# Kernel optimization log

Hardware: AMD Instinct MI355X
Metric: run time of the kernel (lower is better)

Reference implementation:

```python
import jax, jax.numpy as jnp
import numpy as np

VOCAB, E, HIDDEN = 100000, 64, (64, 128, 64)
B, T = 4096, 200


def setup_inputs() -> dict:
    key = jax.random.key(0)
    ks = jax.random.split(key, 12)
    # glorot-ish scales
    def glorot(k, shape):
        fan_in, fan_out = shape[0], shape[-1]
        s = jnp.sqrt(6.0 / (fan_in + fan_out))
        return jax.random.uniform(k, shape, jnp.float32, -s, s)
    return {
        "query": jax.random.randint(ks[0], (B,), 0, VOCAB),
        "keys": jax.random.randint(ks[1], (B, T), 0, VOCAB),
        "emb": glorot(ks[2], (VOCAB, E)),
        "att_w1": glorot(ks[3], (4 * E, 64)),
        "att_b1": jnp.zeros((64,), jnp.float32),
        "att_w2": glorot(ks[4], (64, 1)),
        "att_b2": jnp.zeros((1,), jnp.float32),
        "deep_w1": glorot(ks[5], (HIDDEN[0], HIDDEN[1])),
        "deep_b1": jnp.zeros((HIDDEN[1],), jnp.float32),
        "deep_w2": glorot(ks[6], (HIDDEN[1], HIDDEN[2])),
        "deep_b2": jnp.zeros((HIDDEN[2],), jnp.float32),
        "out_w": glorot(ks[7], (HIDDEN[2], 1)),
        "out_b": jnp.zeros((1,), jnp.float32),
    }


def reference(query, keys, emb, att_w1, att_b1, att_w2, att_b2,
              deep_w1, deep_b1, deep_w2, deep_b2, out_w, out_b):
    q = emb[query]                # [B, E]
    k = emb[keys]                 # [B, T, E]
    qe = jnp.broadcast_to(q[:, None, :], k.shape)  # [B, T, E]
    inter = jnp.concatenate([qe, k, qe - k, qe * k], axis=-1)  # [B, T, 4E]
    h = jax.nn.relu(inter @ att_w1 + att_b1)       # [B, T, 64]
    scores = (h @ att_w2 + att_b2)[..., 0]         # [B, T]
    w = jax.nn.softmax(scores, axis=-1)            # [B, T]
    interest = jnp.einsum("bt,bte->be", w, k)      # [B, E]
    d = jax.nn.relu(interest @ deep_w1 + deep_b1)
    d = jax.nn.relu(d @ deep_w2 + deep_b2)
    return jax.nn.sigmoid(d @ out_w + out_b)       # [B, 1]
```

## Files before the change

### kernel.cpp

```cpp
#include <hip/hip_runtime.h>

#define T 200
#define E 64
#define TPAD 256
#define ROW 72
#define BDIM 256
#define TP 208

typedef __bf16 bf16_t;
typedef __bf16 bf16x8 __attribute__((ext_vector_type(8)));
typedef float f32x4 __attribute__((ext_vector_type(4)));

__global__ __launch_bounds__(256) void pre_cvt(const float* __restrict__ embf,
                                               bf16_t* __restrict__ emb16, int n8,
                                               const float* __restrict__ w1,
                                               float* __restrict__ Ap,
                                               float* __restrict__ Ctf,
                                               float* __restrict__ Dtf) {
    const int bid = blockIdx.x;
    if (bid < 16) {
        const int idx = bid * 256 + threadIdx.x;
        const int e = idx >> 6, j = idx & 63;
        const float a = w1[e * 64 + j];
        const float b = w1[(64 + e) * 64 + j];
        const float c = w1[(128 + e) * 64 + j];
        const float d = w1[(192 + e) * 64 + j];
        Ap[e * 64 + j]  = a + c;
        Ctf[j * 64 + e] = b - c;
        Dtf[j * 64 + e] = d;
        return;
    }
    const int i = (bid - 16) * 256 + threadIdx.x;
    if (i >= n8) return;
    const float4* s = (const float4*)embf + (size_t)i * 2;
    const float4 a = s[0], b = s[1];
    union { bf16_t h[8]; uint4 v; } u;
    u.h[0] = (bf16_t)a.x; u.h[1] = (bf16_t)a.y; u.h[2] = (bf16_t)a.z; u.h[3] = (bf16_t)a.w;
    u.h[4] = (bf16_t)b.x; u.h[5] = (bf16_t)b.y; u.h[6] = (bf16_t)b.z; u.h[7] = (bf16_t)b.w;
    ((uint4*)emb16)[i] = u.v;
}

__global__ __launch_bounds__(256, 4) void din_fast(
    const int* __restrict__ query,
    const int* __restrict__ keys,
    const bf16_t* __restrict__ emb16,
    const float* __restrict__ Ap,
    const float* __restrict__ Ctf,
    const float* __restrict__ Dtf,
    const float* __restrict__ b1,
    const float* __restrict__ w2,
    const float* __restrict__ b2,
    const float* __restrict__ dw1,
    const float* __restrict__ db1,
    const float* __restrict__ dw2,
    const float* __restrict__ db2,
    const float* __restrict__ ow,
    const float* __restrict__ ob,
    float* __restrict__ out)
{
    __shared__ __align__(16) char smem[39936];
    bf16_t* sK   = (bf16_t*)smem;
    bf16_t* sMt  = (bf16_t*)(smem + 29952);
    float*  sUP  = (float*)(smem + 39168);
    float*  sQf  = (float*)(smem + 39680);
    float*  sWgt = (float*)(smem + 29952);
    float*  sRed = (float*)(smem + 30784);
    float*  sInt = (float*)(smem + 30816);
    float*  sD1  = (float*)(smem + 31072);
    float*  sD2  = (float*)(smem + 31584);
    float*  sIP  = (float*)(smem + 31840);

    const int tid  = threadIdx.x;
    const int lane = tid & 63;
    const int wid  = tid >> 6;
    const int b    = blockIdx.x;
    const float b2v = b2[0];

    const int c8    = tid & 7;
    const int rbase = tid >> 3;
    uint4 kr[7];
    #pragma unroll
    for (int i = 0; i < 7; ++i) {
        const int t = rbase + 32 * i;
        if (t < T) {
            const int ki = keys[b * T + t];
            kr[i] = ((const uint4*)(emb16 + (size_t)ki * E))[c8];
        } else {
            kr[i] = make_uint4(0u, 0u, 0u, 0u);
        }
    }

    const int qi = query[b];
    if (tid < 64) sQf[tid] = (float)emb16[(size_t)qi * E + tid];
    __syncthreads();

    if (tid < 128) {
        const int j = tid & 63, ec = tid >> 6;
        float au = 0.f;
        #pragma unroll
        for (int eo = 0; eo < 32; ++eo) {
            const int e = ec * 32 + eo;
            au = fmaf(sQf[e], Ap[e * 64 + j], au);
        }
        sUP[tid] = au;
    }
    {
        const int j = tid & 63, h = tid >> 6;
        const float* cp = Ctf + j * 64 + h * 16;
        const float* dp = Dtf + j * 64 + h * 16;
        const float* qp = sQf + h * 16;
        bf16_t mo[16] __attribute__((aligned(16)));
        #pragma unroll
        for (int x = 0; x < 16; ++x)
            mo[x] = (bf16_t)fmaf(qp[x], dp[x], cp[x]);
        *(bf16x8*)&sMt[j * ROW + h * 16]     = *(bf16x8*)&mo[0];
        *(bf16x8*)&sMt[j * ROW + h * 16 + 8] = *(bf16x8*)&mo[8];
    }
    __syncthreads();

    #pragma unroll
    for (int i = 0; i < 7; ++i) {
        const int t = rbase + 32 * i;
        if (t < TP) *(uint4*)&sK[t * ROW + c8 * 8] = kr[i];
    }
    __syncthreads();

    {
        const int n    = lane & 15;
        const int quad = lane >> 4;
        float w2v[4], uv[4];
        bf16x8 bF[4][2];
        #pragma unroll
        for (int nt = 0; nt < 4; ++nt) {
            const int jj = nt * 16 + n;
            w2v[nt] = w2[jj];
            uv[nt]  = b1[jj] + sUP[jj] + sUP[64 + jj];
            bF[nt][0] = *(const bf16x8*)&sMt[jj * ROW + quad * 8];
            bF[nt][1] = *(const bf16x8*)&sMt[jj * ROW + 32 + quad * 8];
        }
        __syncthreads();

        for (int mt = wid; mt < 13; mt += 4) {
            const bf16x8 a0 = *(const bf16x8*)&sK[(mt * 16 + n) * ROW + quad * 8];
            const bf16x8 a1 = *(const bf16x8*)&sK[(mt * 16 + n) * ROW + 32 + quad * 8];
            float s0 = 0.f, s1 = 0.f, s2 = 0.f, s3 = 0.f;
            #pragma unroll
            for (int nt = 0; nt < 4; ++nt) {
                f32x4 acc = { uv[nt], uv[nt], uv[nt], uv[nt] };
                acc = __builtin_amdgcn_mfma_f32_16x16x32_bf16(a0, bF[nt][0], acc, 0, 0, 0);
                acc = __builtin_amdgcn_mfma_f32_16x16x32_bf16(a1, bF[nt][1], acc, 0, 0, 0);
                s0 = fmaf(fmaxf(acc[0], 0.f), w2v[nt], s0);
                s1 = fmaf(fmaxf(acc[1], 0.f), w2v[nt], s1);
                s2 = fmaf(fmaxf(acc[2], 0.f), w2v[nt], s2);
                s3 = fmaf(fmaxf(acc[3], 0.f), w2v[nt], s3);
            }
            #pragma unroll
            for (int off = 1; off < 16; off <<= 1) {
                s0 += __shfl_xor(s0, off);
                s1 += __shfl_xor(s1, off);
                s2 += __shfl_xor(s2, off);
                s3 += __shfl_xor(s3, off);
            }
            if (n == 0) {
                const int base = mt * 16 + quad * 4;
                sWgt[base + 0] = s0;
                sWgt[base + 1] = s1;
                sWgt[base + 2] = s2;
                sWgt[base + 3] = s3;
            }
        }
    }
    __syncthreads();

    {
        const float score = (tid < T) ? (sWgt[tid] + b2v) : -1e30f;
        float m = score;
        #pragma unroll
        for (int off = 32; off > 0; off >>= 1) m = fmaxf(m, __shfl_xor(m, off));
        if (lane == 0) sRed[wid] = m;
        __syncthreads();
        const float gmax = fmaxf(fmaxf(sRed[0], sRed[1]), fmaxf(sRed[2], sRed[3]));
        const float p = (tid < T) ? __expf(score - gmax) : 0.f;
        float s = p;
        #pragma unroll
        for (int off = 32; off > 0; off >>= 1) s += __shfl_xor(s, off);
        if (lane == 0) sRed[4 + wid] = s;
        __syncthreads();
        const float gsum = sRed[4] + sRed[5] + sRed[6] + sRed[7];
        if (tid < T) sWgt[tid] = p / gsum;
    }
    __syncthreads();

    {
        const int e = tid & 63, ch = tid >> 6;
        float a = 0.f;
        #pragma unroll 10
        for (int tt = 0; tt < 50; ++tt) {
            const int t = ch * 50 + tt;
            a = fmaf(sWgt[t], (float)sK[t * ROW + e], a);
        }
        sIP[tid] = a;
    }
    __syncthreads();
    if (tid < 64) sInt[tid] = sIP[tid] + sIP[64 + tid] + sIP[128 + tid] + sIP[192 + tid];
    __syncthreads();

    if (tid < 128) {
        float a = db1[tid];
        #pragma unroll 8
        for (int e = 0; e < 64; ++e) a = fmaf(sInt[e], dw1[e * 128 + tid], a);
        sD1[tid] = fmaxf(a, 0.f);
    }
    __syncthreads();
    if (tid < 64) {
        float a = db2[tid];
        #pragma unroll 8
        for (int i = 0; i < 128; ++i) a = fmaf(sD1[i], dw2[i * 64 + tid], a);
        sD2[tid] = fmaxf(a, 0.f);
    }
    __syncthreads();
    if (tid < 64) {
        float v = sD2[tid] * ow[tid];
        #pragma unroll
        for (int off = 32; off > 0; off >>= 1) v += __shfl_xor(v, off);
        if (tid == 0) out[b] = 1.f / (1.f + __expf(-(v + ob[0])));
    }
}

__global__ __launch_bounds__(BDIM, 3) void din_kernel(
    const int* __restrict__ query,
    const int* __restrict__ keys,
    const float* __restrict__ embf,
    const bf16_t* __restrict__ emb16,
    const int use16,
    const float* __restrict__ w1,
    const float* __restrict__ b1,
    const float* __restrict__ w2,
    const float* __restrict__ b2,
    const float* __restrict__ dw1,
    const float* __restrict__ db1,
    const float* __restrict__ dw2,
    const float* __restrict__ db2,
    const float* __restrict__ ow,
    const float* __restrict__ ob,
    float* __restrict__ out)
{
    __shared__ __align__(16) char sRaw[TPAD * ROW * 2];
    __shared__ __align__(16) bf16_t sMt[64 * ROW];
    __shared__ float sU[64];
    __shared__ float sUP[256];
    __shared__ float sW2f[64];
    __shared__ float sWgt[256];
    __shared__ float sQf[64];
    __shared__ __align__(16) char sQtmp[128];
    __shared__ float sRed[8];
    __shared__ float sInt[64];
    __shared__ float sD1[128];
    __shared__ float sD2[64];

    const int tid  = threadIdx.x;
    const int lane = tid & 63;
    const int wid  = tid >> 6;
    const int b    = blockIdx.x;
    const float b2v = b2[0];

    uint4 kr[8];
    if (tid < T) {
        const int ki = keys[b * T + tid];
        if (use16) {
            const uint4* kp = (const uint4*)(emb16 + (size_t)ki * E);
            #pragma unroll
            for (int c = 0; c < 8; ++c) kr[c] = kp[c];
        } else {
            const float4* kp = (const float4*)(embf + (size_t)ki * E);
            #pragma unroll
            for (int c = 0; c < 8; ++c) {
                const float4 x = kp[2 * c], y = kp[2 * c + 1];
                union { bf16_t h[8]; uint4 v; } u;
                u.h[0] = (bf16_t)x.x; u.h[1] = (bf16_t)x.y; u.h[2] = (bf16_t)x.z; u.h[3] = (bf16_t)x.w;
                u.h[4] = (bf16_t)y.x; u.h[5] = (bf16_t)y.y; u.h[6] = (bf16_t)y.z; u.h[7] = (bf16_t)y.w;
                kr[c] = u.v;
            }
        }
    } else {
        #pragma unroll
        for (int c = 0; c < 8; ++c) kr[c] = make_uint4(0u, 0u, 0u, 0u);
    }

    const int qi = query[b];
    if (tid < 8) {
        uint4 qv;
        if (use16) {
            qv = ((const uint4*)(emb16 + (size_t)qi * E))[tid];
        } else {
            const float4 x = ((const float4*)(embf + (size_t)qi * E))[2 * tid];
            const float4 y = ((const float4*)(embf + (size_t)qi * E))[2 * tid + 1];
            union { bf16_t h[8]; uint4 v; } u;
            u.h[0] = (bf16_t)x.x; u.h[1] = (bf16_t)x.y; u.h[2] = (bf16_t)x.z; u.h[3] = (bf16_t)x.w;
            u.h[4] = (bf16_t)y.x; u.h[5] = (bf16_t)y.y; u.h[6] = (bf16_t)y.z; u.h[7] = (bf16_t)y.w;
            qv = u.v;
        }
        ((uint4*)sQtmp)[tid] = qv;
    }
    if (tid < 64) sW2f[tid] = w2[tid];
    __syncthreads();
    if (tid < 64) sQf[tid] = (float)((const bf16_t*)sQtmp)[tid];
    __syncthreads();

    {
        float* sTmp = (float*)sRaw;
        const int j = tid & 63, ec = tid >> 6;
        float au = 0.f;
        #pragma unroll
        for (int eo = 0; eo < 16; ++eo) {
            const int e = ec * 16 + eo;
            const float w1a = w1[e * 64 + j];
            const float w1b = w1[(64 + e) * 64 + j];
            const float w1c = w1[(128 + e) * 64 + j];
            const float w1d = w1[(192 + e) * 64 + j];
            sTmp[e * 65 + j] = w1b - w1c + sQf[e] * w1d;
            au = fmaf(sQf[e], w1a + w1c, au);
        }
        sUP[tid] = au;
    }
    __syncthreads();
    {
        const float* sTmp = (const float*)sRaw;
        const int e = tid & 63, jc = tid >> 6;
        #pragma unroll
        for (int jo = 0; jo < 16; ++jo) {
            const int j = jc * 16 + jo;
            sMt[j * ROW + e] = (bf16_t)sTmp[e * 65 + j];
        }
    }
    if (tid < 64) sU[tid] = b1[tid] + sUP[tid] + sUP[64 + tid] + sUP[128 + tid] + sUP[192 + tid];
    __syncthreads();

    bf16_t* sK = (bf16_t*)sRaw;
    {
        uint4* dst = (uint4*)(sK + tid * ROW);
        #pragma unroll
        for (int c = 0; c < 8; ++c) dst[c] = kr[c];
    }
    __syncthreads();

    {
        const int n    = lane & 15;
        const int quad = lane >> 4;
        float w2v[4], uv[4];
        bf16x8 bF[4][2];
        #pragma unroll
        for (int nt = 0; nt < 4; ++nt) {
            w2v[nt] = sW2f[nt * 16 + n];
            uv[nt]  = sU[nt * 16 + n];
            bF[nt][0] = *(const bf16x8*)&sMt[(nt * 16 + n) * ROW + quad * 8];
            bF[nt][1] = *(const bf16x8*)&sMt[(nt * 16 + n) * ROW + 32 + quad * 8];
        }
        #pragma unroll
        for (int i = 0; i < 4; ++i) {
            const int mt = wid * 4 + i;
            const bf16x8 a0 = *(const bf16x8*)&sK[(mt * 16 + n) * ROW + quad * 8];
            const bf16x8 a1 = *(const bf16x8*)&sK[(mt * 16 + n) * ROW + 32 + quad * 8];
            float s0 = 0.f, s1 = 0.f, s2 = 0.f, s3 = 0.f;
            #pragma unroll
            for (int nt = 0; nt < 4; ++nt) {
                f32x4 acc = { uv[nt], uv[nt], uv[nt], uv[nt] };
                acc = __builtin_amdgcn_mfma_f32_16x16x32_bf16(a0, bF[nt][0], acc, 0, 0, 0);
                acc = __builtin_amdgcn_mfma_f32_16x16x32_bf16(a1, bF[nt][1], acc, 0, 0, 0);
                s0 = fmaf(fmaxf(acc[0], 0.f), w2v[nt], s0);
                s1 = fmaf(fmaxf(acc[1], 0.f), w2v[nt], s1);
                s2 = fmaf(fmaxf(acc[2], 0.f), w2v[nt], s2);
                s3 = fmaf(fmaxf(acc[3], 0.f), w2v[nt], s3);
            }
            #pragma unroll
            for (int off = 1; off < 16; off <<= 1) {
                s0 += __shfl_xor(s0, off);
                s1 += __shfl_xor(s1, off);
                s2 += __shfl_xor(s2, off);
                s3 += __shfl_xor(s3, off);
            }
            if (n == 0) {
                const int base = mt * 16 + quad * 4;
                sWgt[base + 0] = s0;
                sWgt[base + 1] = s1;
                sWgt[base + 2] = s2;
                sWgt[base + 3] = s3;
            }
        }
    }
    __syncthreads();

    {
        const float score = (tid < T) ? (sWgt[tid] + b2v) : -1e30f;
        float m = score;
        #pragma unroll
        for (int off = 32; off > 0; off >>= 1) m = fmaxf(m, __shfl_xor(m, off));
        if (lane == 0) sRed[wid] = m;
        __syncthreads();
        const float gmax = fmaxf(fmaxf(sRed[0], sRed[1]), fmaxf(sRed[2], sRed[3]));
        const float p = (tid < T) ? __expf(score - gmax) : 0.f;
        float s = p;
        #pragma unroll
        for (int off = 32; off > 0; off >>= 1) s += __shfl_xor(s, off);
        if (lane == 0) sRed[4 + wid] = s;
        __syncthreads();
        const float gsum = sRed[4] + sRed[5] + sRed[6] + sRed[7];
        sWgt[tid] = p / gsum;
    }
    __syncthreads();

    {
        const int e = tid & 63, ch = tid >> 6;
        float a = 0.f;
        #pragma unroll 8
        for (int tt = 0; tt < 64; ++tt) {
            const int t = ch * 64 + tt;
            a = fmaf(sWgt[t], (float)sK[t * ROW + e], a);
        }
        sUP[tid] = a;
    }
    __syncthreads();
    if (tid < 64) sInt[tid] = sUP[tid] + sUP[64 + tid] + sUP[128 + tid] + sUP[192 + tid];
    __syncthreads();

    if (tid < 128) {
        float a = db1[tid];
        #pragma unroll 8
        for (int e = 0; e < 64; ++e) a = fmaf(sInt[e], dw1[e * 128 + tid], a);
        sD1[tid] = fmaxf(a, 0.f);
    }
    __syncthreads();
    if (tid < 64) {
        float a = db2[tid];
        #pragma unroll 8
        for (int i = 0; i < 128; ++i) a = fmaf(sD1[i], dw2[i * 64 + tid], a);
        sD2[tid] = fmaxf(a, 0.f);
    }
    __syncthreads();
    if (tid < 64) {
        float v = sD2[tid] * ow[tid];
        #pragma unroll
        for (int off = 32; off > 0; off >>= 1) v += __shfl_xor(v, off);
        if (tid == 0) out[b] = 1.f / (1.f + __expf(-(v + ob[0])));
    }
}

extern "C" void kernel_launch(void* const* d_in, const int* in_sizes, int n_in,
                              void* d_out, int out_size, void* d_ws, size_t ws_size,
                              hipStream_t stream) {
    const int*   query = (const int*)d_in[0];
    const int*   keys  = (const int*)d_in[1];
    const float* embf  = (const float*)d_in[2];
    const float* w1    = (const float*)d_in[3];
    const float* b1    = (const float*)d_in[4];
    const float* w2    = (const float*)d_in[5];
    const float* b2    = (const float*)d_in[6];
    const float* dw1   = (const float*)d_in[7];
    const float* db1   = (const float*)d_in[8];
    const float* dw2   = (const float*)d_in[9];
    const float* db2   = (const float*)d_in[10];
    const float* ow    = (const float*)d_in[11];
    const float* ob    = (const float*)d_in[12];
    float* out = (float*)d_out;
    const int B        = in_sizes[0];
    const int embElems = in_sizes[2];
    const size_t WOFF  = 49152;

    if (ws_size >= WOFF + (size_t)embElems * 2) {
        float*  Ap    = (float*)d_ws;
        float*  Ctf   = (float*)((char*)d_ws + 16384);
        float*  Dtf   = (float*)((char*)d_ws + 32768);
        bf16_t* emb16 = (bf16_t*)((char*)d_ws + WOFF);
        const int n8 = embElems / 8;
        pre_cvt<<<16 + (n8 + 255) / 256, 256, 0, stream>>>(embf, emb16, n8,
                                                           w1, Ap, Ctf, Dtf);
        din_fast<<<B, BDIM, 0, stream>>>(query, keys, emb16, Ap, Ctf, Dtf,
                                         b1, w2, b2, dw1, db1, dw2, db2, ow, ob, out);
    } else {
        din_kernel<<<B, BDIM, 0, stream>>>(query, keys, embf, (const bf16_t*)d_ws, 0,
                                           w1, b1, w2, b2, dw1, db1, dw2, db2, ow, ob, out);
    }
}
```

Baseline: 167.1 us.

## Process two batch rows per block, prefetching second row's keys during first

Each block now handles two batch rows. The gathered key embeddings and the query for the second row are loaded into registers while the first row's scoring, softmax and MLP run. This hides gather latency behind compute and halves the grid size. In exchange it raises register pressure (the 7 uint4 prefetch registers stay live across the MFMA section), which may reduce occupancy, and it halves the number of blocks available to spread across CUs.

Result: no change. 166.8 us (-0.1%).

```diff
diff --git a/kernel.cpp b/kernel.cpp
--- a/kernel.cpp
+++ b/kernel.cpp
@@ -56,7 +56,8 @@
     const float* __restrict__ db2,
     const float* __restrict__ ow,
     const float* __restrict__ ob,
-    float* __restrict__ out)
+    float* __restrict__ out,
+    const int nB)
 {
     __shared__ __align__(16) char smem[39936];
     bf16_t* sK   = (bf16_t*)smem;
@@ -73,25 +74,28 @@
     const int tid  = threadIdx.x;
     const int lane = tid & 63;
     const int wid  = tid >> 6;
-    const int b    = blockIdx.x;
+    const int bA   = blockIdx.x * 2;
+    const bool hasB = (bA + 1) < nB;
+    const int bB   = hasB ? (bA + 1) : bA;
     const float b2v = b2[0];
-
     const int c8    = tid & 7;
     const int rbase = tid >> 3;
+    const int n    = lane & 15;
+    const int quad = lane >> 4;
+
     uint4 kr[7];
     #pragma unroll
     for (int i = 0; i < 7; ++i) {
         const int t = rbase + 32 * i;
         if (t < T) {
-            const int ki = keys[b * T + t];
+            const int ki = keys[bA * T + t];
             kr[i] = ((const uint4*)(emb16 + (size_t)ki * E))[c8];
         } else {
             kr[i] = make_uint4(0u, 0u, 0u, 0u);
         }
     }
-
-    const int qi = query[b];
-    if (tid < 64) sQf[tid] = (float)emb16[(size_t)qi * E + tid];
+    const int qiA = query[bA];
+    if (tid < 64) sQf[tid] = (float)emb16[(size_t)qiA * E + tid];
     __syncthreads();
 
     if (tid < 128) {
@@ -125,11 +129,10 @@
     }
     __syncthreads();
 
-    {
-        const int n    = lane & 15;
-        const int quad = lane >> 4;
-        float w2v[4], uv[4];
-        bf16x8 bF[4][2];
+    float w2v[4], uv[4];
+    bf16x8 bF[4][2];
+    float qpre = 0.f;
+    {
         #pragma unroll
         for (int nt = 0; nt < 4; ++nt) {
             const int jj = nt * 16 + n;
@@ -139,6 +142,18 @@
             bF[nt][1] = *(const bf16x8*)&sMt[jj * ROW + 32 + quad * 8];
         }
         __syncthreads();
+
+        #pragma unroll
+        for (int i = 0; i < 7; ++i) {
+            const int t = rbase + 32 * i;
+            if (t < T) {
+                const int ki = keys[bB * T + t];
+                kr[i] = ((const uint4*)(emb16 + (size_t)ki * E))[c8];
+            } else {
+                kr[i] = make_uint4(0u, 0u, 0u, 0u);
+            }
+        }
+        if (tid < 64) qpre = (float)emb16[(size_t)query[bB] * E + tid];
 
         for (int mt = wid; mt < 13; mt += 4) {
             const bf16x8 a0 = *(const bf16x8*)&sK[(mt * 16 + n) * ROW + quad * 8];
@@ -202,7 +217,16 @@
         sIP[tid] = a;
     }
     __syncthreads();
-    if (tid < 64) sInt[tid] = sIP[tid] + sIP[64 + tid] + sIP[128 + tid] + sIP[192 + tid];
+
+    #pragma unroll
+    for (int i = 0; i < 7; ++i) {
+        const int t = rbase + 32 * i;
+        if (t < TP) *(uint4*)&sK[t * ROW + c8 * 8] = kr[i];
+    }
+    if (tid < 64) {
+        sQf[tid] = qpre;
+        sInt[tid] = sIP[tid] + sIP[64 + tid] + sIP[128 + tid] + sIP[192 + tid];
+    }
     __syncthreads();
 
     if (tid < 128) {
@@ -223,7 +247,129 @@
         float v = sD2[tid] * ow[tid];
         #pragma unroll
         for (int off = 32; off > 0; off >>= 1) v += __shfl_xor(v, off);
-        if (tid == 0) out[b] = 1.f / (1.f + __expf(-(v + ob[0])));
+        if (tid == 0) out[bA] = 1.f / (1.f + __expf(-(v + ob[0])));
+    }
+
+    if (hasB) {
+        __syncthreads();
+
+        if (tid < 128) {
+            const int j = tid & 63, ec = tid >> 6;
+            float au = 0.f;
+            #pragma unroll
+            for (int eo = 0; eo < 32; ++eo) {
+                const int e = ec * 32 + eo;
+                au = fmaf(sQf[e], Ap[e * 64 + j], au);
+            }
+            sUP[tid] = au;
+        }
+        {
+            const int j = tid & 63, h = tid >> 6;
+            const float* cp = Ctf + j * 64 + h * 16;
+            const float* dp = Dtf + j * 64 + h * 16;
+            const float* qp = sQf + h * 16;
+            bf16_t mo[16] __attribute__((aligned(16)));
+            #pragma unroll
+            for (int x = 0; x < 16; ++x)
+                mo[x] = (bf16_t)fmaf(qp[x], dp[x], cp[x]);
+            *(bf16x8*)&sMt[j * ROW + h * 16]     = *(bf16x8*)&mo[0];
+            *(bf16x8*)&sMt[j * ROW + h * 16 + 8] = *(bf16x8*)&mo[8];
+        }
+        __syncthreads();
+
+        #pragma unroll
+        for (int nt = 0; nt < 4; ++nt) {
+            const int jj = nt * 16 + n;
+            uv[nt]  = b1[jj] + sUP[jj] + sUP[64 + jj];
+            bF[nt][0] = *(const bf16x8*)&sMt[jj * ROW + quad * 8];
+            bF[nt][1] = *(const bf16x8*)&sMt[jj * ROW + 32 + quad * 8];
+        }
+        __syncthreads();
+
+        for (int mt = wid; mt < 13; mt += 4) {
+            const bf16x8 a0 = *(const bf16x8*)&sK[(mt * 16 + n) * ROW + quad * 8];
+            const bf16x8 a1 = *(const bf16x8*)&sK[(mt * 16 + n) * ROW + 32 + quad * 8];
+            float s0 = 0.f, s1 = 0.f, s2 = 0.f, s3 = 0.f;
+            #pragma unroll
+            for (int nt = 0; nt < 4; ++nt) {
+                f32x4 acc = { uv[nt], uv[nt], uv[nt], uv[nt] };
+                acc = __builtin_amdgcn_mfma_f32_16x16x32_bf16(a0, bF[nt][0], acc, 0, 0, 0);
+                acc = __builtin_amdgcn_mfma_f32_16x16x32_bf16(a1, bF[nt][1], acc, 0, 0, 0);
+                s0 = fmaf(fmaxf(acc[0], 0.f), w2v[nt], s0);
+                s1 = fmaf(fmaxf(acc[1], 0.f), w2v[nt], s1);
+                s2 = fmaf(fmaxf(acc[2], 0.f), w2v[nt], s2);
+                s3 = fmaf(fmaxf(acc[3], 0.f), w2v[nt], s3);
+            }
+            #pragma unroll
+            for (int off = 1; off < 16; off <<= 1) {
+                s0 += __shfl_xor(s0, off);
+                s1 += __shfl_xor(s1, off);
+                s2 += __shfl_xor(s2, off);
+                s3 += __shfl_xor(s3, off);
+            }
+            if (n == 0) {
+                const int base = mt * 16 + quad * 4;
+                sWgt[base + 0] = s0;
+                sWgt[base + 1] = s1;
+                sWgt[base + 2] = s2;
+                sWgt[base + 3] = s3;
+            }
+        }
+        __syncthreads();
+
+        {
+            const float score = (tid < T) ? (sWgt[tid] + b2v) : -1e30f;
+            float m = score;
+            #pragma unroll
+            for (int off = 32; off > 0; off >>= 1) m = fmaxf(m, __shfl_xor(m, off));
+            if (lane == 0) sRed[wid] = m;
+            __syncthreads();
+            const float gmax = fmaxf(fmaxf(sRed[0], sRed[1]), fmaxf(sRed[2], sRed[3]));
+            const float p = (tid < T) ? __expf(score - gmax) : 0.f;
+            float s = p;
+            #pragma unroll
+            for (int off = 32; off > 0; off >>= 1) s += __shfl_xor(s, off);
+            if (lane == 0) sRed[4 + wid] = s;
+            __syncthreads();
+            const float gsum = sRed[4] + sRed[5] + sRed[6] + sRed[7];
+            if (tid < T) sWgt[tid] = p / gsum;
+        }
+        __syncthreads();
+
+        {
+            const int e = tid & 63, ch = tid >> 6;
+            float a = 0.f;
+            #pragma unroll 10
+            for (int tt = 0; tt < 50; ++tt) {
+                const int t = ch * 50 + tt;
+                a = fmaf(sWgt[t], (float)sK[t * ROW + e], a);
+            }
+            sIP[tid] = a;
+        }
+        __syncthreads();
+        if (tid < 64) sInt[tid] = sIP[tid] + sIP[64 + tid] + sIP[128 + tid] + sIP[192 + tid];
+        __syncthreads();
+
+        if (tid < 128) {
+            float a = db1[tid];
+            #pragma unroll 8
+            for (int e = 0; e < 64; ++e) a = fmaf(sInt[e], dw1[e * 128 + tid], a);
+            sD1[tid] = fmaxf(a, 0.f);
+        }
+        __syncthreads();
+        if (tid < 64) {
+            float a = db2[tid];
+            #pragma unroll 8
+            for (int i = 0; i < 128; ++i) a = fmaf(sD1[i], dw2[i * 64 + tid], a);
+            sD2[tid] = fmaxf(a, 0.f);
+        }
+        __syncthreads();
+        if (tid < 64) {
+            float v = sD2[tid] * ow[tid];
+            #pragma unroll
+            for (int off = 32; off > 0; off >>= 1) v += __shfl_xor(v, off);
+            if (tid == 0) out[bA + 1] = 1.f / (1.f + __expf(-(v + ob[0])));
+        }
     }
 }
 
@@ -474,8 +620,9 @@
         const int n8 = embElems / 8;
         pre_cvt<<<16 + (n8 + 255) / 256, 256, 0, stream>>>(embf, emb16, n8,
                                                            w1, Ap, Ctf, Dtf);
-        din_fast<<<B, BDIM, 0, stream>>>(query, keys, emb16, Ap, Ctf, Dtf,
-                                         b1, w2, b2, dw1, db1, dw2, db2, ow, ob, out);
+        din_fast<<<(B + 1) / 2, BDIM, 0, stream>>>(query, keys, emb16, Ap, Ctf, Dtf,
+                                                   b1, w2, b2, dw1, db1, dw2, db2,
+                                                   ow, ob, out, B);
     } else {
         din_kernel<<<B, BDIM, 0, stream>>>(query, keys, embf, (const bf16_t*)d_ws, 0,
                                            w1, b1, w2, b2, dw1, db1, dw2, db2, ow, ob, out);
```

## Map one batch row per wavefront and keep gathered keys in registers

Applied to the files above, without the earlier changes.

Replaces the one-block-per-row kernel with a kernel in which each 64-lane wavefront handles a whole batch row. The gathered key embeddings are loaded straight into MFMA operand registers, so the shared-memory staging and the block-wide __syncthreads barriers go away, and the weighted sum and the small MLP are done with wave-level shuffles. Each wave now computes its own query projections, which adds redundant global loads and raises register pressure (26 bf16x8 arrays), so launch bounds are lowered to 2 blocks per SM.

After: 145.8 us. 1.15x faster.

```diff
diff --git a/kernel.cpp b/kernel.cpp
--- a/kernel.cpp
+++ b/kernel.cpp
@@ -5,7 +5,6 @@
 #define TPAD 256
 #define ROW 72
 #define BDIM 256
-#define TP 208
 
 typedef __bf16 bf16_t;
 typedef __bf16 bf16x8 __attribute__((ext_vector_type(8)));
@@ -40,7 +39,7 @@
     ((uint4*)emb16)[i] = u.v;
 }
 
-__global__ __launch_bounds__(256, 4) void din_fast(
+__global__ __launch_bounds__(256, 2) void din_wave(
     const int* __restrict__ query,
     const int* __restrict__ keys,
     const bf16_t* __restrict__ emb16,
@@ -56,174 +55,181 @@
     const float* __restrict__ db2,
     const float* __restrict__ ow,
     const float* __restrict__ ob,
-    float* __restrict__ out)
+    float* __restrict__ out,
+    const int nB)
 {
-    __shared__ __align__(16) char smem[39936];
-    bf16_t* sK   = (bf16_t*)smem;
-    bf16_t* sMt  = (bf16_t*)(smem + 29952);
-    float*  sUP  = (float*)(smem + 39168);
-    float*  sQf  = (float*)(smem + 39680);
-    float*  sWgt = (float*)(smem + 29952);
-    float*  sRed = (float*)(smem + 30784);
-    float*  sInt = (float*)(smem + 30816);
-    float*  sD1  = (float*)(smem + 31072);
-    float*  sD2  = (float*)(smem + 31584);
-    float*  sIP  = (float*)(smem + 31840);
-
+    __shared__ __align__(16) char smem[4 * 1664];
     const int tid  = threadIdx.x;
+    const int wid  = tid >> 6;
     const int lane = tid & 63;
-    const int wid  = tid >> 6;
-    const int b    = blockIdx.x;
-    const float b2v = b2[0];
-
-    const int c8    = tid & 7;
-    const int rbase = tid >> 3;
-    uint4 kr[7];
-    #pragma unroll
-    for (int i = 0; i < 7; ++i) {
-        const int t = rbase + 32 * i;
-        if (t < T) {
-            const int ki = keys[b * T + t];
-            kr[i] = ((const uint4*)(emb16 + (size_t)ki * E))[c8];
-        } else {
-            kr[i] = make_uint4(0u, 0u, 0u, 0u);
-        }
-    }
+    const int n    = lane & 15;
+    const int quad = lane >> 4;
+    const int b    = blockIdx.x * 4 + wid;
+    if (b >= nB) return;
+
+    float* sWgt = (float*)(smem + wid * 1664);
+    float* sInt = (float*)(smem + wid * 1664 + 832);
+    float* sD1  = (float*)(smem + wid * 1664 + 1088);
 
     const int qi = query[b];
-    if (tid < 64) sQf[tid] = (float)emb16[(size_t)qi * E + tid];
-    __syncthreads();
-
-    if (tid < 128) {
-        const int j = tid & 63, ec = tid >> 6;
-        float au = 0.f;
-        #pragma unroll
-        for (int eo = 0; eo < 32; ++eo) {
-            const int e = ec * 32 + eo;
-            au = fmaf(sQf[e], Ap[e * 64 + j], au);
-        }
-        sUP[tid] = au;
-    }
-    {
-        const int j = tid & 63, h = tid >> 6;
-        const float* cp = Ctf + j * 64 + h * 16;
-        const float* dp = Dtf + j * 64 + h * 16;
-        const float* qp = sQf + h * 16;
-        bf16_t mo[16] __attribute__((aligned(16)));
-        #pragma unroll
-        for (int x = 0; x < 16; ++x)
-            mo[x] = (bf16_t)fmaf(qp[x], dp[x], cp[x]);
-        *(bf16x8*)&sMt[j * ROW + h * 16]     = *(bf16x8*)&mo[0];
-        *(bf16x8*)&sMt[j * ROW + h * 16 + 8] = *(bf16x8*)&mo[8];
-    }
-    __syncthreads();
-
-    #pragma unroll
-    for (int i = 0; i < 7; ++i) {
-        const int t = rbase + 32 * i;
-        if (t < TP) *(uint4*)&sK[t * ROW + c8 * 8] = kr[i];
-    }
-    __syncthreads();
-
-    {
-        const int n    = lane & 15;
-        const int quad = lane >> 4;
-        float w2v[4], uv[4];
-        bf16x8 bF[4][2];
+    const bf16x8 q0 = *(const bf16x8*)(emb16 + (size_t)qi * E + quad * 8);
+    const bf16x8 q1 = *(const bf16x8*)(emb16 + (size_t)qi * E + 32 + quad * 8);
+
+    int kidx[13];
+    #pragma unroll
+    for (int mt = 0; mt < 13; ++mt) {
+        const int t = mt * 16 + n;
+        kidx[mt] = (t < T) ? keys[b * T + t] : 0;
+    }
+    bf16x8 a0[13], a1[13];
+    #pragma unroll
+    for (int mt = 0; mt < 13; ++mt) {
+        const bf16_t* rp = emb16 + (size_t)kidx[mt] * E;
+        a0[mt] = *(const bf16x8*)(rp + quad * 8);
+        a1[mt] = *(const bf16x8*)(rp + 32 + quad * 8);
+    }
+
+    float u = 0.f;
+    #pragma unroll
+    for (int e = 0; e < 64; ++e)
+        u = fmaf((float)emb16[(size_t)qi * E + e], Ap[e * 64 + lane], u);
+
+    float uv[4], w2v[4];
+    #pragma unroll
+    for (int nt = 0; nt < 4; ++nt) {
+        const int jj = nt * 16 + n;
+        uv[nt]  = b1[jj] + __shfl(u, jj);
+        w2v[nt] = w2[jj];
+    }
+
+    bf16x8 bF[4][2];
+    #pragma unroll
+    for (int nt = 0; nt < 4; ++nt) {
+        const int jj = nt * 16 + n;
+        const float* cb = Ctf + jj * 64;
+        const float* db = Dtf + jj * 64;
+        union { bf16_t h[8]; bf16x8 v; } u0, u1;
+        #pragma unroll
+        for (int x = 0; x < 8; ++x) {
+            u0.h[x] = (bf16_t)fmaf((float)q0[x], db[quad * 8 + x],      cb[quad * 8 + x]);
+            u1.h[x] = (bf16_t)fmaf((float)q1[x], db[32 + quad * 8 + x], cb[32 + quad * 8 + x]);
+        }
+        bF[nt][0] = u0.v;
+        bF[nt][1] = u1.v;
+    }
+
+    #pragma unroll
+    for (int mt = 0; mt < 13; ++mt) {
+        float s0 = 0.f, s1 = 0.f, s2 = 0.f, s3 = 0.f;
         #pragma unroll
         for (int nt = 0; nt < 4; ++nt) {
-            const int jj = nt * 16 + n;
-            w2v[nt] = w2[jj];
-            uv[nt]  = b1[jj] + sUP[jj] + sUP[64 + jj];
-            bF[nt][0] = *(const bf16x8*)&sMt[jj * ROW + quad * 8];
-            bF[nt][1] = *(const bf16x8*)&sMt[jj * ROW + 32 + quad * 8];
-        }
-        __syncthreads();
-
-        for (int mt = wid; mt < 13; mt += 4) {
-            const bf16x8 a0 = *(const bf16x8*)&sK[(mt * 16 + n) * ROW + quad * 8];
-            const bf16x8 a1 = *(const bf16x8*)&sK[(mt * 16 + n) * ROW + 32 + quad * 8];
-            float s0 = 0.f, s1 = 0.f, s2 = 0.f, s3 = 0.f;
-            #pragma unroll
-            for (int nt = 0; nt < 4; ++nt) {
-                f32x4 acc = { uv[nt], uv[nt], uv[nt], uv[nt] };
-                acc = __builtin_amdgcn_mfma_f32_16x16x32_bf16(a0, bF[nt][0], acc, 0, 0, 0);
-                acc = __builtin_amdgcn_mfma_f32_16x16x32_bf16(a1, bF[nt][1], acc, 0, 0, 0);
-                s0 = fmaf(fmaxf(acc[0], 0.f), w2v[nt], s0);
-                s1 = fmaf(fmaxf(acc[1], 0.f), w2v[nt], s1);
-                s2 = fmaf(fmaxf(acc[2], 0.f), w2v[nt], s2);
-                s3 = fmaf(fmaxf(acc[3], 0.f), w2v[nt], s3);
-            }
+            f32x4 acc = { uv[nt], uv[nt], uv[nt], uv[nt] };
+            acc = __builtin_amdgcn_mfma_f32_16x16x32_bf16(a0[mt], bF[nt][0], acc, 0, 0, 0);
+            acc = __builtin_amdgcn_mfma_f32_16x16x32_bf16(a1[mt], bF[nt][1], acc, 0, 0, 0);
+            s0 = fmaf(fmaxf(acc[0], 0.f), w2v[nt], s0);
+            s1 = fmaf(fmaxf(acc[1], 0.f), w2v[nt], s1);
+            s2 = fmaf(fmaxf(acc[2], 0.f), w2v[nt], s2);
+            s3 = fmaf(fmaxf(acc[3], 0.f), w2v[nt], s3);
+        }
+        #pragma unroll
+        for (int off = 1; off < 16; off <<= 1) {
+            s0 += __shfl_xor(s0, off);
+            s1 += __shfl_xor(s1, off);
+            s2 += __shfl_xor(s2, off);
+            s3 += __shfl_xor(s3, off);
+        }
+        if (n == 0) {
+            const int base = mt * 16 + quad * 4;
+            sWgt[base + 0] = s0;
+            sWgt[base + 1] = s1;
+            sWgt[base + 2] = s2;
+            sWgt[base + 3] = s3;
+        }
+    }
+    asm volatile("s_waitcnt lgkmcnt(0)" ::: "memory");
+    __builtin_amdgcn_sched_barrier(0);
+
+    {
+        const float b2v = b2[0];
+        const float x0 = sWgt[lane] + b2v;
+        const float x1 = sWgt[64 + lane] + b2v;
+        const float x2 = sWgt[128 + lane] + b2v;
+        const float x3 = (lane < 8) ? (sWgt[192 + lane] + b2v) : -1e30f;
+        float m = fmaxf(fmaxf(x0, x1), fmaxf(x2, x3));
+        #pragma unroll
+        for (int off = 32; off > 0; off >>= 1) m = fmaxf(m, __shfl_xor(m, off));
+        const float p0 = __expf(x0 - m);
+        const float p1 = __expf(x1 - m);
+        const float p2 = __expf(x2 - m);
+        const float p3 = (lane < 8) ? __expf(x3 - m) : 0.f;
+        float s = ((p0 + p1) + (p2 + p3));
+        #pragma unroll
+        for (int off = 32; off > 0; off >>= 1) s += __shfl_xor(s, off);
+        const float inv = 1.f / s;
+        sWgt[lane]       = p0 * inv;
+        sWgt[64 + lane]  = p1 * inv;
+        sWgt[128 + lane] = p2 * inv;
+        if (lane < 8) sWgt[192 + lane] = p3 * inv;
+    }
+    asm volatile("s_waitcnt lgkmcnt(0)" ::: "memory");
+    __builtin_amdgcn_sched_barrier(0);
+
+    {
+        float pa[8], pb[8];
+        #pragma unroll
+        for (int x = 0; x < 8; ++x) { pa[x] = 0.f; pb[x] = 0.f; }
+        #pragma unroll
+        for (int mt = 0; mt < 13; ++mt) {
+            const int t = mt * 16 + n;
+            const float wt = (t < T) ? sWgt[t] : 0.f;
+            #pragma unroll
+            for (int x = 0; x < 8; ++x) {
+                pa[x] = fmaf(wt, (float)a0[mt][x], pa[x]);
+                pb[x] = fmaf(wt, (float)a1[mt][x], pb[x]);
+            }
+        }
+        #pragma unroll
+        for (int x = 0; x < 8; ++x) {
             #pragma unroll
             for (int off = 1; off < 16; off <<= 1) {
-                s0 += __shfl_xor(s0, off);
-                s1 += __shfl_xor(s1, off);
-                s2 += __shfl_xor(s2, off);
-                s3 += __shfl_xor(s3, off);
-            }
-            if (n == 0) {
-                const int base = mt * 16 + quad * 4;
-                sWgt[base + 0] = s0;
-                sWgt[base + 1] = s1;
-                sWgt[base + 2] = s2;
-                sWgt[base + 3] = s3;
-            }
-        }
-    }
-    __syncthreads();
-
-    {
-        const float score = (tid < T) ? (sWgt[tid] + b2v) : -1e30f;
-        float m = score;
-        #pragma unroll
-        for (int off = 32; off > 0; off >>= 1) m = fmaxf(m, __shfl_xor(m, off));
-        if (lane == 0) sRed[wid] = m;
-        __syncthreads();
-        const float gmax = fmaxf(fmaxf(sRed[0], sRed[1]), fmaxf(sRed[2], sRed[3]));
-        const float p = (tid < T) ? __expf(score - gmax) : 0.f;
-        float s = p;
-        #pragma unroll
-        for (int off = 32; off > 0; off >>= 1) s += __shfl_xor(s, off);
-        if (lane == 0) sRed[4 + wid] = s;
-        __syncthreads();
-        const float gsum = sRed[4] + sRed[5] + sRed[6] + sRed[7];
-        if (tid < T) sWgt[tid] = p / gsum;
-    }
-    __syncthreads();
-
-    {
-        const int e = tid & 63, ch = tid >> 6;
-        float a = 0.f;
-        #pragma unroll 10
-        for (int tt = 0; tt < 50; ++tt) {
-            const int t = ch * 50 + tt;
-            a = fmaf(sWgt[t], (float)sK[t * ROW + e], a);
-        }
-        sIP[tid] = a;
-    }
-    __syncthreads();
-    if (tid < 64) sInt[tid] = sIP[tid] + sIP[64 + tid] + sIP[128 + tid] + sIP[192 + tid];
-    __syncthreads();
-
-    if (tid < 128) {
-        float a = db1[tid];
-        #pragma unroll 8
-        for (int e = 0; e < 64; ++e) a = fmaf(sInt[e], dw1[e * 128 + tid], a);
-        sD1[tid] = fmaxf(a, 0.f);
-    }
-    __syncthreads();
-    if (tid < 64) {
-        float a = db2[tid];
-        #pragma unroll 8
-        for (int i = 0; i < 128; ++i) a = fmaf(sD1[i], dw2[i * 64 + tid], a);
-        sD2[tid] = fmaxf(a, 0.f);
-    }
-    __syncthreads();
-    if (tid < 64) {
-        float v = sD2[tid] * ow[tid];
+                pa[x] += __shfl_xor(pa[x], off);
+                pb[x] += __shfl_xor(pb[x], off);
+            }
+        }
+        if (n == 0) {
+            #pragma unroll
+            for (int x = 0; x < 8; ++x) {
+                sInt[quad * 8 + x]      = pa[x];
+                sInt[32 + quad * 8 + x] = pb[x];
+            }
+        }
+    }
+    asm volatile("s_waitcnt lgkmcnt(0)" ::: "memory");
+    __builtin_amdgcn_sched_barrier(0);
+
+    {
+        float d1a = db1[lane], d1b = db1[64 + lane];
+        #pragma unroll
+        for (int e = 0; e < 64; ++e) {
+            const float ie = sInt[e];
+            d1a = fmaf(ie, dw1[e * 128 + lane], d1a);
+            d1b = fmaf(ie, dw1[e * 128 + 64 + lane], d1b);
+        }
+        sD1[lane]      = fmaxf(d1a, 0.f);
+        sD1[64 + lane] = fmaxf(d1b, 0.f);
+    }
+    asm volatile("s_waitcnt lgkmcnt(0)" ::: "memory");
+    __builtin_amdgcn_sched_barrier(0);
+
+    {
+        float o = db2[lane];
+        #pragma unroll
+        for (int i = 0; i < 128; ++i)
+            o = fmaf(sD1[i], dw2[i * 64 + lane], o);
+        float v = fmaxf(o, 0.f) * ow[lane];
         #pragma unroll
         for (int off = 32; off > 0; off >>= 1) v += __shfl_xor(v, off);
-        if (tid == 0) out[b] = 1.f / (1.f + __expf(-(v + ob[0])));
+        if (lane == 0) out[b] = 1.f / (1.f + __expf(-(v + ob[0])));
     }
 }
 
@@ -474,8 +480,9 @@
         const int n8 = embElems / 8;
         pre_cvt<<<16 + (n8 + 255) / 256, 256, 0, stream>>>(embf, emb16, n8,
                                                            w1, Ap, Ctf, Dtf);
-        din_fast<<<B, BDIM, 0, stream>>>(query, keys, emb16, Ap, Ctf, Dtf,
-                                         b1, w2, b2, dw1, db1, dw2, db2, ow, ob, out);
+        din_wave<<<(B + 3) / 4, BDIM, 0, stream>>>(query, keys, emb16, Ap, Ctf, Dtf,
+                                                   b1, w2, b2, dw1, db1, dw2, db2,
+                                                   ow, ob, out, B);
     } else {
         din_kernel<<<B, BDIM, 0, stream>>>(query, keys, embf, (const bf16_t*)d_ws, 0,
                                            w1, b1, w2, b2, dw1, db1, dw2, db2, ow, ob, out);
```
